# Kernel optimization log

Hardware: AMD Instinct MI355X
Metric: run time of the kernel (lower is better)

## Reference

```python
import math
import jax, jax.numpy as jnp
import numpy as np

B, T, E, H, A, NF = 8, 512, 1024, 16, 64, 64
HS = E // H
MLP = 4 * E

def _sinpos(t, dim):
    half = dim // 2
    freqs = jnp.exp(-math.log(10000.0) / (half - 1) * jnp.arange(half, dtype=jnp.float32))
    args = t.astype(jnp.float32)[:, None] * freqs[None, :]
    return jnp.concatenate([jnp.sin(args), jnp.cos(args)], axis=-1)

def _ada_ln(x, temb, w, b):
    # DiT-style adaLN: shift/scale modulate the normed x, alpha gates the branch
    h = jax.nn.silu(temb) @ w + b                      # [B, 3E]
    shift, scale, alpha = jnp.split(h, 3, axis=-1)
    mu = jnp.mean(x, axis=-1, keepdims=True)
    var = jnp.var(x, axis=-1, keepdims=True)
    xn = (x - mu) * jax.lax.rsqrt(var + 1e-5)
    return xn * (1.0 + scale[:, None, :]) + shift[:, None, :], alpha[:, None, :]

def _split_heads(x):
    b, n, c = x.shape
    return x.reshape(b, n, H, c // H).transpose(0, 2, 1, 3)

def _agent_attn(q, k, v, agents, qw, qb, kw, kb, vw, vb, ow, ob):
    # two-stage agent attention: agents attend to k/v, then q attends to agent context
    hs = q.shape[-1]
    inv = 1.0 / math.sqrt(hs)
    qa = agents[0] @ qw + qb                           # [H, A, hs] (shared across batch)
    ka = k @ kw + kb                                   # [B, H, N, hs]
    va = v @ vw + vb
    s1 = jax.nn.softmax(jnp.einsum('hax,bhnx->bhan', qa, ka) * inv, axis=-1)
    c1 = jnp.einsum('bhan,bhnx->bhax', s1, va)         # [B, H, A, hs]
    s2 = jax.nn.softmax(jnp.einsum('bhnx,bhax->bhna', q, c1) * inv, axis=-1)
    c2 = jnp.einsum('bhna,bhax->bhnx', s2, c1)         # [B, H, N, hs]
    b, h, n, _ = c2.shape
    return c2.transpose(0, 2, 1, 3).reshape(b, n, h * hs) @ ow + ob

def _conv1d(x, w, b):
    y = jax.lax.conv_general_dilated(x, w, (1,), [(1, 1)],
                                     dimension_numbers=('NCH', 'OIH', 'NCH'))
    return y + b[None, :, None]

def _fourier(x, low_freq=1, factor=1):
    b, t, d = x.shape
    xf = jnp.fft.rfft(x, axis=1)
    if t % 2 == 0:
        xf = xf[:, low_freq:-1]
        f = jnp.fft.rfftfreq(t)[low_freq:-1]
    else:
        xf = xf[:, low_freq:]
        f = jnp.fft.rfftfreq(t)[low_freq:]
    k = int(factor * math.log(xf.shape[1]))
    _, idx = jax.lax.top_k(jnp.moveaxis(jnp.abs(xf), 1, -1), k)    # [b, d, k]
    idx = jnp.moveaxis(idx, -1, 1)                                 # [b, k, d]
    xf_top = jnp.take_along_axis(xf, idx, axis=1)                  # [b, k, d] complex
    f_top = f.astype(jnp.float32)[idx]                             # [b, k, d]
    xf2 = jnp.concatenate([xf_top, jnp.conj(xf_top)], axis=1)      # [b, 2k, d]
    f2 = jnp.concatenate([f_top, -f_top], axis=1)[:, :, None, :]
    tt = jnp.arange(t, dtype=jnp.float32)[None, None, :, None]
    amp = jnp.abs(xf2)[:, :, None, :]
    phase = jnp.angle(xf2)[:, :, None, :]
    return jnp.sum(amp * jnp.cos(2.0 * math.pi * f2 * tt + phase), axis=1)

def _forward(x, encoder_output, timestep,
             ln1_w, ln1_b, ln11_w, ln11_b, ln2_w, ln2_b,
             a1_qkv_w, a1_qkv_b, a1_agq_w, a1_agq_b, a1_agk_w, a1_agk_b,
             a1_agv_w, a1_agv_b, a1_ago_w, a1_ago_b, a1_agents, a1_proj_w, a1_proj_b,
             a2_q_w, a2_q_b, a2_kv_w, a2_kv_b, a2_agq_w, a2_agq_b, a2_agk_w, a2_agk_b,
             a2_agv_w, a2_agv_b, a2_ago_w, a2_ago_b, a2_agents, a2_proj_w, a2_proj_b,
             tr_c1_w, tr_c1_b, tr_c2_w, tr_c2_b,
             mlp_w1, mlp_b1, mlp_w2, mlp_b2,
             pr_w, pr_b, lin_w, lin_b):
    temb = _sinpos(timestep, E)
    # self-attention (FullAttention with agent bottleneck)
    n1, al1 = _ada_ln(x, temb, ln1_w, ln1_b)
    q, k, v = jnp.split(n1 @ a1_qkv_w + a1_qkv_b, 3, axis=-1)
    y = _agent_attn(_split_heads(q), _split_heads(k), _split_heads(v), a1_agents,
                    a1_agq_w, a1_agq_b, a1_agk_w, a1_agk_b, a1_agv_w, a1_agv_b,
                    a1_ago_w, a1_ago_b)
    x = x + al1 * (y @ a1_proj_w + a1_proj_b)
    # cross-attention
    n11, al11 = _ada_ln(x, temb, ln11_w, ln11_b)
    qc = n11 @ a2_q_w + a2_q_b
    kc, vc = jnp.split(encoder_output @ a2_kv_w + a2_kv_b, 2, axis=-1)
    y = _agent_attn(_split_heads(qc), _split_heads(kc), _split_heads(vc), a2_agents,
                    a2_agq_w, a2_agq_b, a2_agk_w, a2_agk_b, a2_agv_w, a2_agv_b,
                    a2_ago_w, a2_ago_b)
    x = x + al11 * (y @ a2_proj_w + a2_proj_b)
    # 1x1 conv over channel dim (n_channel) then split into trend/seasonal inputs
    p = jnp.einsum('bce,oc->boe', x, pr_w) + pr_b[None, :, None]
    x1, x2 = jnp.split(p, 2, axis=1)
    h = jax.nn.gelu(_conv1d(x1, tr_c1_w, tr_c1_b), approximate=False)   # [B, 3, E]
    h = _conv1d(h.transpose(0, 2, 1), tr_c2_w, tr_c2_b)                 # [B, NF, 3]
    lin = jnp.arange(1, T + 1, dtype=jnp.float32) / (T + 1)
    poly = jnp.stack([lin ** (p_ + 1) for p_ in range(3)], axis=0)      # [3, T]
    trend = jnp.einsum('bnp,pt->btn', h, poly)                          # [B, T, NF]
    # seasonal branch: top-k Fourier extrapolation
    season = _fourier(x2)
    # MLP
    n2, al2 = _ada_ln(x, temb, ln2_w, ln2_b)
    mlp = jax.nn.gelu(n2 @ mlp_w1 + mlp_b1, approximate=False) @ mlp_w2 + mlp_b2
    x = x + al2 * mlp
    m = jnp.mean(x, axis=1, keepdims=True)
    return (x - m, m @ lin_w + lin_b, trend, season)

def setup_inputs():
    ks = iter(jax.random.split(jax.random.key(0), 64))
    def nrm(shape, s=0.02):
        return jax.random.normal(next(ks), shape, dtype=jnp.float32) * s
    z = lambda *s: jnp.zeros(s, jnp.float32)
    return dict(
        x=nrm((B, T, E), 1.0),
        encoder_output=nrm((B, T, E), 1.0),
        timestep=jax.random.randint(next(ks), (B,), 0, 1000),
        ln1_w=nrm((E, 3 * E)), ln1_b=z(3 * E),
        ln11_w=nrm((E, 3 * E)), ln11_b=z(3 * E),
        ln2_w=nrm((E, 3 * E)), ln2_b=z(3 * E),
        a1_qkv_w=nrm((E, 3 * E)), a1_qkv_b=z(3 * E),
        a1_agq_w=nrm((HS, HS)), a1_agq_b=z(HS),
        a1_agk_w=nrm((HS, HS)), a1_agk_b=z(HS),
        a1_agv_w=nrm((HS, HS)), a1_agv_b=z(HS),
        a1_ago_w=nrm((E, E)), a1_ago_b=z(E),
        a1_agents=nrm((1, H, A, HS), 1.0),
        a1_proj_w=nrm((E, E)), a1_proj_b=z(E),
        a2_q_w=nrm((E, E)), a2_q_b=z(E),
        a2_kv_w=nrm((E, 2 * E)), a2_kv_b=z(2 * E),
        a2_agq_w=nrm((HS, HS)), a2_agq_b=z(HS),
        a2_agk_w=nrm((HS, HS)), a2_agk_b=z(HS),
        a2_agv_w=nrm((HS, HS)), a2_agv_b=z(HS),
        a2_ago_w=nrm((E, E)), a2_ago_b=z(E),
        a2_agents=nrm((1, H, A, HS), 1.0),
        a2_proj_w=nrm((E, E)), a2_proj_b=z(E),
        tr_c1_w=nrm((3, T, 3)), tr_c1_b=z(3),
        tr_c2_w=nrm((NF, E, 3)), tr_c2_b=z(NF),
        mlp_w1=nrm((E, MLP)), mlp_b1=z(MLP),
        mlp_w2=nrm((MLP, E)), mlp_b2=z(E),
        pr_w=nrm((2 * T, T)), pr_b=z(2 * T),
        lin_w=nrm((E, NF)), lin_b=z(NF),
    )

def reference(x, encoder_output, timestep,
              ln1_w, ln1_b, ln11_w, ln11_b, ln2_w, ln2_b,
              a1_qkv_w, a1_qkv_b, a1_agq_w, a1_agq_b, a1_agk_w, a1_agk_b,
              a1_agv_w, a1_agv_b, a1_ago_w, a1_ago_b, a1_agents, a1_proj_w, a1_proj_b,
              a2_q_w, a2_q_b, a2_kv_w, a2_kv_b, a2_agq_w, a2_agq_b, a2_agk_w, a2_agk_b,
              a2_agv_w, a2_agv_b, a2_ago_w, a2_ago_b, a2_agents, a2_proj_w, a2_proj_b,
              tr_c1_w, tr_c1_b, tr_c2_w, tr_c2_b,
              mlp_w1, mlp_b1, mlp_w2, mlp_b2,
              pr_w, pr_b, lin_w, lin_b):
    return _forward(x, encoder_output, timestep,
                    ln1_w, ln1_b, ln11_w, ln11_b, ln2_w, ln2_b,
                    a1_qkv_w, a1_qkv_b, a1_agq_w, a1_agq_b, a1_agk_w, a1_agk_b,
                    a1_agv_w, a1_agv_b, a1_ago_w, a1_ago_b, a1_agents, a1_proj_w, a1_proj_b,
                    a2_q_w, a2_q_b, a2_kv_w, a2_kv_b, a2_agq_w, a2_agq_b, a2_agk_w, a2_agk_b,
                    a2_agv_w, a2_agv_b, a2_ago_w, a2_ago_b, a2_agents, a2_proj_w, a2_proj_b,
                    tr_c1_w, tr_c1_b, tr_c2_w, tr_c2_b,
                    mlp_w1, mlp_b1, mlp_w2, mlp_b2,
                    pr_w, pr_b, lin_w, lin_b)
```

## Files before the change

kernel.cpp:

```cpp
#include <hip/hip_runtime.h>
#include <hip/hip_bf16.h>

using bf16 = __hip_bfloat16;
typedef __attribute__((ext_vector_type(8))) short short8;
typedef __attribute__((ext_vector_type(4))) float floatx4;

constexpr int kB = 8, kT = 512, kE = 1024, kH = 16, kA = 64, kNF = 64, kHS = 64;
constexpr int kMLP = 4096, kT2 = 1024, kNFREQ = 255, kKTOP = 5;

constexpr int TAG_F32 = 0, TAG_BF16 = 1, TAG_AUTO = 2;

constexpr long BOFF_XC    = 0;
constexpr long BOFF_SMALL = 16777216;
constexpr long BOFF_FLAG  = 21137408;
constexpr long BOFF_WREG  = 21137472;
constexpr long BOFF_ACT   = 42108992;
constexpr long WS_NEED    = BOFF_ACT + 67108864;

constexpr long WR_Q   = 0;
constexpr long WR_KV  = 4194304;
constexpr long WR_AGO = 12582912;
constexpr long WR_PRJ = 16777216;
constexpr long WR_W1  = 0;
constexpr long WR_W2  = 8388608;

constexpr long AC_N1   = 0;
constexpr long AC_QBUF = 16777216;
constexpr long AC_KV   = 33554432;
constexpr long AC_KA   = 0;
constexpr long AC_VA   = 8388608;
constexpr long AC_ATT  = 33554432;
constexpr long AC_Y2   = 50331648;
constexpr long AC_P    = 0;
constexpr long AC_RE   = 33554432;
constexpr long AC_IM   = 41910272;
constexpr long AC_N1B  = 0;
constexpr long AC_HID  = 8388608;

constexpr long F_TS = 0, F_AD1 = 8192, F_AD11 = 32768, F_AD2 = 57344, F_QA = 81920,
               F_C1 = 147456, F_H2 = 671744, F_G1 = 673280, F_MB = 697856,
               F_TRE = 706048, F_TIM = 747008, F_TIX = 787968, F_TRIG = 828928;

constexpr long O0 = 0, O1 = 4194304, O2 = 4194816, O3 = 4456960;

__device__ inline float bf2f(bf16 h) {
    unsigned short u = *(unsigned short*)&h;
    return __uint_as_float((unsigned)u << 16);
}
__device__ inline unsigned short bfbits(bf16 b) { return *(unsigned short*)&b; }
__device__ inline float gelu_f(float x) {
    return 0.5f * x * (1.0f + erff(x * 0.7071067811865476f));
}
__device__ inline float4 load4f(const float* p) { return *(const float4*)p; }
__device__ inline float4 load4bf(const bf16* p) {
    ushort4 u = *(const ushort4*)p;
    float4 r;
    r.x = __uint_as_float((unsigned)u.x << 16);
    r.y = __uint_as_float((unsigned)u.y << 16);
    r.z = __uint_as_float((unsigned)u.z << 16);
    r.w = __uint_as_float((unsigned)u.w << 16);
    return r;
}
__device__ inline float4 load4auto(const void* p, long idx, bool isF32) {
    if (isF32) return load4f((const float*)p + idx);
    return load4bf((const bf16*)p + idx);
}
__device__ inline float ld1auto(const void* p, long idx, bool isF32) {
    if (isF32) return ((const float*)p)[idx];
    return bf2f(((const bf16*)p)[idx]);
}
__device__ inline void st1auto(void* p, long idx, bool isF32, float v) {
    if (isF32) ((float*)p)[idx] = v;
    else       ((bf16*)p)[idx] = __float2bfloat16(v);
}
__device__ inline float ldc1(const float* p) { return *p; }
__device__ inline float ldc1(const bf16* p) { return bf2f(*p); }
__device__ inline void stc1(float* p, float v) { *p = v; }
__device__ inline void stc1(bf16* p, float v) { *p = __float2bfloat16(v); }

__device__ inline void blockReduce2(float& a, float& b, float* sm) {
    #pragma unroll
    for (int m = 32; m > 0; m >>= 1) { a += __shfl_down(a, m); b += __shfl_down(b, m); }
    int w = threadIdx.x >> 6;
    if ((threadIdx.x & 63) == 0) { sm[w] = a; sm[4 + w] = b; }
    __syncthreads();
    a = sm[0] + sm[1] + sm[2] + sm[3];
    b = sm[4] + sm[5] + sm[6] + sm[7];
    __syncthreads();
}

__global__ void k_detect(const unsigned short* __restrict__ xraw, int* __restrict__ flag) {
    int tid = threadIdx.x;
    unsigned short h = xraw[2 * tid];
    float v = __uint_as_float((unsigned)h << 16);
    float av = fabsf(v);
    if (!(av == av)) av = 1e30f;
    __shared__ float red[4];
    for (int m = 32; m > 0; m >>= 1) av = fmaxf(av, __shfl_down(av, m));
    if ((tid & 63) == 0) red[tid >> 6] = av;
    __syncthreads();
    if (tid == 0) {
        float mx = fmaxf(fmaxf(red[0], red[1]), fmaxf(red[2], red[3]));
        flag[0] = (mx < 1e3f) ? 0 : 1;
    }
}

__global__ void k_temb(const int* __restrict__ ts, float* __restrict__ out) {
    int b = blockIdx.x, i = threadIdx.x;
    float t = (float)ts[b];
    const float rate = (float)(-9.210340371976184 / 511.0);
    float f = expf(rate * (float)i);
    float arg = t * f;
    float sv = sinf(arg), cv = cosf(arg);
    out[(long)b * kE + i]        = sv / (1.f + expf(-sv));
    out[(long)b * kE + 512 + i]  = cv / (1.f + expf(-cv));
}

__global__ void k_castin(const void* __restrict__ in, float* __restrict__ out,
                         const int* __restrict__ DF) {
    bool f = DF[0] != 0;
    long i = ((long)blockIdx.x * 256 + threadIdx.x) * 4;
    float4 v = load4auto(in, i, f);
    *(float4*)(out + i) = v;
}

__global__ __launch_bounds__(256) void k_wtf(const void* __restrict__ W, float* __restrict__ WT,
                                             int K, int Ntot, int c0,
                                             const int* __restrict__ DF) {
    bool f = DF[0] != 0;
    __shared__ float tile[32][33];
    int n0 = blockIdx.x * 32, k0 = blockIdx.y * 32;
    int tx = threadIdx.x & 31, ty = threadIdx.x >> 5;
    #pragma unroll
    for (int i = 0; i < 4; i++) {
        int k = ty + i * 8;
        tile[k][tx] = ld1auto(W, (long)(k0 + k) * Ntot + c0 + n0 + tx, f);
    }
    __syncthreads();
    #pragma unroll
    for (int i = 0; i < 4; i++) {
        int n = ty + i * 8;
        WT[(long)(n0 + n) * K + k0 + tx] = tile[tx][n];
    }
}

__global__ __launch_bounds__(256) void k_wt(const void* __restrict__ W, bf16* __restrict__ WT,
                                            int K, int N, const int* __restrict__ DF) {
    bool f = DF[0] != 0;
    __shared__ float tile[32][33];
    int n0 = blockIdx.x * 32, k0 = blockIdx.y * 32;
    int tx = threadIdx.x & 31, ty = threadIdx.x >> 5;
    #pragma unroll
    for (int i = 0; i < 4; i++) {
        int k = ty + i * 8;
        tile[k][tx] = ld1auto(W, (long)(k0 + k) * N + n0 + tx, f);
    }
    __syncthreads();
    #pragma unroll
    for (int i = 0; i < 4; i++) {
        int n = ty + i * 8;
        WT[(long)(n0 + n) * K + k0 + tx] = __float2bfloat16(tile[tx][n]);
    }
}

__global__ __launch_bounds__(256) void k_adalnf(const float* __restrict__ X,
                                                const float* __restrict__ AD,
                                                float* __restrict__ N) {
    int row = blockIdx.x;
    int b = row / kT;
    const float* xr = X + (long)row * kE;
    int tid = threadIdx.x;
    float4 xv = *(const float4*)(xr + tid * 4);
    float s  = xv.x + xv.y + xv.z + xv.w;
    float sq = xv.x * xv.x + xv.y * xv.y + xv.z * xv.z + xv.w * xv.w;
    __shared__ float sm[8];
    blockReduce2(s, sq, sm);
    float mu  = s * (1.f / kE);
    float var = sq * (1.f / kE) - mu * mu;
    float rstd = rsqrtf(fmaxf(var, 0.f) + 1e-5f);
    const float* ad = AD + (long)b * 3 * kE;
    float* nr = N + (long)row * kE;
    float xs[4] = {xv.x, xv.y, xv.z, xv.w};
    #pragma unroll
    for (int j = 0; j < 4; j++) {
        int e = tid * 4 + j;
        float xn = (xs[j] - mu) * rstd;
        nr[e] = xn * (1.f + ad[kE + e]) + ad[e];
    }
}

__global__ __launch_bounds__(256) void k_adaln(const float* __restrict__ X,
                                               const float* __restrict__ AD,
                                               bf16* __restrict__ N) {
    int row = blockIdx.x;
    int b = row / kT;
    const float* xr = X + (long)row * kE;
    int tid = threadIdx.x;
    float4 xv = *(const float4*)(xr + tid * 4);
    float s  = xv.x + xv.y + xv.z + xv.w;
    float sq = xv.x * xv.x + xv.y * xv.y + xv.z * xv.z + xv.w * xv.w;
    __shared__ float sm[8];
    blockReduce2(s, sq, sm);
    float mu  = s * (1.f / kE);
    float var = sq * (1.f / kE) - mu * mu;
    float rstd = rsqrtf(fmaxf(var, 0.f) + 1e-5f);
    const float* ad = AD + (long)b * 3 * kE;
    bf16* nr = N + (long)row * kE;
    float xs[4] = {xv.x, xv.y, xv.z, xv.w};
    #pragma unroll
    for (int j = 0; j < 4; j++) {
        int e = tid * 4 + j;
        float xn = (xs[j] - mu) * rstd;
        nr[e] = __float2bfloat16(xn * (1.f + ad[kE + e]) + ad[e]);
    }
}

template <typename TC>
__global__ __launch_bounds__(256) void k_mfma32(
    const float* __restrict__ A, int lda,
    const float* __restrict__ WT,
    TC* __restrict__ C, int ldc,
    int M, int N, int K,
    const void* __restrict__ bias, int bTag, long biasOff,
    const float* __restrict__ alpha, int alphaStride, int rowsPerB,
    const int* __restrict__ DF) {
    constexpr int BK = 32, PAD = 8;
    __shared__ bf16 Ah[128][BK + PAD], Al[128][BK + PAD];
    __shared__ bf16 Bh[128][BK + PAD], Bl[128][BK + PAD];
    int tid = threadIdx.x;
    int wave = tid >> 6, lane = tid & 63;
    int bm = blockIdx.y * 128, bn = blockIdx.x * 128;
    int wm = (wave >> 1) * 64, wn = (wave & 1) * 64;
    int lm = lane & 15, quad = lane >> 4;
    floatx4 acc[4][4] = {};
    int sRow = tid >> 1, sCol = (tid & 1) * 16;
    const float* ag = A  + (long)(bm + sRow) * lda + sCol;
    const float* bg = WT + (long)(bn + sRow) * K   + sCol;
    for (int k0 = 0; k0 < K; k0 += BK) {
        #pragma unroll
        for (int i = 0; i < 4; i++) {
            float4 v = *(const float4*)(ag + k0 + i * 4);
            bf16 h0 = __float2bfloat16(v.x), h1 = __float2bfloat16(v.y);
            bf16 h2 = __float2bfloat16(v.z), h3 = __float2bfloat16(v.w);
            bf16 l0 = __float2bfloat16(v.x - bf2f(h0));
            bf16 l1 = __float2bfloat16(v.y - bf2f(h1));
            bf16 l2 = __float2bfloat16(v.z - bf2f(h2));
            bf16 l3 = __float2bfloat16(v.w - bf2f(h3));
            ushort4 hv = {bfbits(h0), bfbits(h1), bfbits(h2), bfbits(h3)};
            ushort4 lv = {bfbits(l0), bfbits(l1), bfbits(l2), bfbits(l3)};
            *(ushort4*)&Ah[sRow][sCol + i * 4] = hv;
            *(ushort4*)&Al[sRow][sCol + i * 4] = lv;
        }
        #pragma unroll
        for (int i = 0; i < 4; i++) {
            float4 v = *(const float4*)(bg + k0 + i * 4);
            bf16 h0 = __float2bfloat16(v.x), h1 = __float2bfloat16(v.y);
            bf16 h2 = __float2bfloat16(v.z), h3 = __float2bfloat16(v.w);
            bf16 l0 = __float2bfloat16(v.x - bf2f(h0));
            bf16 l1 = __float2bfloat16(v.y - bf2f(h1));
            bf16 l2 = __float2bfloat16(v.z - bf2f(h2));
            bf16 l3 = __float2bfloat16(v.w - bf2f(h3));
            ushort4 hv = {bfbits(h0), bfbits(h1), bfbits(h2), bfbits(h3)};
            ushort4 lv = {bfbits(l0), bfbits(l1), bfbits(l2), bfbits(l3)};
            *(ushort4*)&Bh[sRow][sCol + i * 4] = hv;
            *(ushort4*)&Bl[sRow][sCol + i * 4] = lv;
        }
        __syncthreads();
        short8 ahf[4], alf[4], bhf[4], blf[4];
        #pragma unroll
        for (int mi = 0; mi < 4; mi++) {
            ahf[mi] = *(const short8*)&Ah[wm + mi * 16 + lm][quad * 8];
            alf[mi] = *(const short8*)&Al[wm + mi * 16 + lm][quad * 8];
        }
        #pragma unroll
        for (int ni = 0; ni < 4; ni++) {
            bhf[ni] = *(const short8*)&Bh[wn + ni * 16 + lm][quad * 8];
            blf[ni] = *(const short8*)&Bl[wn + ni * 16 + lm][quad * 8];
        }
        #pragma unroll
        for (int mi = 0; mi < 4; mi++)
            #pragma unroll
            for (int ni = 0; ni < 4; ni++) {
                acc[mi][ni] = __builtin_amdgcn_mfma_f32_16x16x32_bf16(ahf[mi], bhf[ni], acc[mi][ni], 0, 0, 0);
                acc[mi][ni] = __builtin_amdgcn_mfma_f32_16x16x32_bf16(ahf[mi], blf[ni], acc[mi][ni], 0, 0, 0);
                acc[mi][ni] = __builtin_amdgcn_mfma_f32_16x16x32_bf16(alf[mi], bhf[ni], acc[mi][ni], 0, 0, 0);
            }
        __syncthreads();
    }
    bool f32f = DF[0] != 0;
    bool bF = (bTag == TAG_F32) || (bTag == TAG_AUTO && f32f);
    #pragma unroll
    for (int ni = 0; ni < 4; ni++) {
        int col = bn + wn + ni * 16 + lm;
        float cb = bias ? ld1auto(bias, biasOff + col, bF) : 0.f;
        #pragma unroll
        for (int mi = 0; mi < 4; mi++) {
            #pragma unroll
            for (int reg = 0; reg < 4; reg++) {
                int row = bm + wm + mi * 16 + quad * 4 + reg;
                float v = acc[mi][ni][reg] + cb;
                TC* cp = C + (long)row * ldc + col;
                if (alpha) {
                    const float* al = alpha + (long)(row / rowsPerB) * alphaStride + col;
                    v = ldc1(cp) + al[0] * v;
                }
                stc1(cp, v);
            }
        }
    }
}

template <typename TC>
static void mgemm32(hipStream_t s, const float* A, int lda, const float* WT,
                    TC* C, int ldc, int M, int N, int K,
                    const void* bias, int bTag, long biasOff,
                    const float* alpha, int alphaStride, int rowsPerB, const int* DF) {
    dim3 g(N / 128, M / 128);
    k_mfma32<TC><<<g, 256, 0, s>>>(A, lda, WT, C, ldc, M, N, K,
                                   bias, bTag, biasOff, alpha, alphaStride, rowsPerB, DF);
}

template <typename TC>
__global__ __launch_bounds__(256) void k_mfma(
    const bf16* __restrict__ A, int lda,
    const bf16* __restrict__ WT,
    TC* __restrict__ C, int ldc,
    int M, int N, int K,
    const void* __restrict__ bias, int bTag, int act,
    const float* __restrict__ alpha, int alphaStride, int rowsPerB,
    const int* __restrict__ DF) {
    constexpr int BK = 64, PAD = 8;
    __shared__ bf16 As[128][BK + PAD];
    __shared__ bf16 Bs[128][BK + PAD];
    int tid = threadIdx.x;
    int wave = tid >> 6, lane = tid & 63;
    int bm = blockIdx.y * 128, bn = blockIdx.x * 128;
    int wm = (wave >> 1) * 64, wn = (wave & 1) * 64;
    int lm = lane & 15, quad = lane >> 4;
    floatx4 acc[4][4] = {};
    int sRow = tid >> 1, sCol = (tid & 1) * 32;
    const bf16* ag = A  + (long)(bm + sRow) * lda + sCol;
    const bf16* bg = WT + (long)(bn + sRow) * K   + sCol;
    for (int k0 = 0; k0 < K; k0 += BK) {
        #pragma unroll
        for (int i = 0; i < 4; i++)
            *(float4*)&As[sRow][sCol + i * 8] = *(const float4*)(ag + k0 + i * 8);
        #pragma unroll
        for (int i = 0; i < 4; i++)
            *(float4*)&Bs[sRow][sCol + i * 8] = *(const float4*)(bg + k0 + i * 8);
        __syncthreads();
        #pragma unroll
        for (int kk = 0; kk < BK; kk += 32) {
            short8 af[4], bf[4];
            #pragma unroll
            for (int mi = 0; mi < 4; mi++)
                af[mi] = *(const short8*)&As[wm + mi * 16 + lm][kk + quad * 8];
            #pragma unroll
            for (int ni = 0; ni < 4; ni++)
                bf[ni] = *(const short8*)&Bs[wn + ni * 16 + lm][kk + quad * 8];
            #pragma unroll
            for (int mi = 0; mi < 4; mi++)
                #pragma unroll
                for (int ni = 0; ni < 4; ni++)
                    acc[mi][ni] = __builtin_amdgcn_mfma_f32_16x16x32_bf16(
                        af[mi], bf[ni], acc[mi][ni], 0, 0, 0);
        }
        __syncthreads();
    }
    bool f32f = DF[0] != 0;
    bool bF = (bTag == TAG_F32) || (bTag == TAG_AUTO && f32f);
    #pragma unroll
    for (int ni = 0; ni < 4; ni++) {
        int col = bn + wn + ni * 16 + lm;
        float cb = bias ? ld1auto(bias, col, bF) : 0.f;
        #pragma unroll
        for (int mi = 0; mi < 4; mi++) {
            #pragma unroll
            for (int reg = 0; reg < 4; reg++) {
                int row = bm + wm + mi * 16 + quad * 4 + reg;
                float v = acc[mi][ni][reg] + cb;
                TC* cp = C + (long)row * ldc + col;
                if (alpha) {
                    const float* al = alpha + (long)(row / rowsPerB) * alphaStride + col;
                    v = ldc1(cp) + al[0] * v;
                } else if (act == 1) {
                    v = gelu_f(v);
                }
                stc1(cp, v);
            }
        }
    }
}

template <typename TC>
static void mgemm(hipStream_t s, const bf16* A, int lda, const bf16* WT,
                  TC* C, int ldc, int M, int N, int K,
                  const void* bias, int bTag, int act,
                  const float* alpha, int alphaStride, int rowsPerB, const int* DF) {
    dim3 g(N / 128, M / 128);
    k_mfma<TC><<<g, 256, 0, s>>>(A, lda, WT, C, ldc, M, N, K,
                                 bias, bTag, act, alpha, alphaStride, rowsPerB, DF);
}

template <typename TC>
__global__ __launch_bounds__(256) void k_gemm(
    const void* __restrict__ Ab, int aTag, int lda, long bsA,
    const void* __restrict__ Wb, int wTag, int ldw, long bsW,
    TC* __restrict__ Cb, int ldc, long bsC,
    int M, int N, int K,
    const void* __restrict__ bias, int bTag, int biasRow, int act,
    const float* __restrict__ alpha, int alphaStride, int rowsPerB,
    const int* __restrict__ DF) {
    __shared__ float As[16][68];
    __shared__ float Bs[16][68];
    bool f32f = DF[0] != 0;
    bool aF = (aTag == TAG_F32) || (aTag == TAG_AUTO && f32f);
    bool wF = (wTag == TAG_F32) || (wTag == TAG_AUTO && f32f);
    bool bF = (bTag == TAG_F32) || (bTag == TAG_AUTO && f32f);
    TC* Cbase = Cb + (long)blockIdx.z * bsC;
    long aBase = (long)blockIdx.z * bsA;
    long wBase = (long)blockIdx.z * bsW;
    int tid = threadIdx.x;
    int bm = blockIdx.y, bn = blockIdx.x;
    int tx = tid & 15, ty = tid >> 4;
    int arow = tid >> 2, acol = (tid & 3) * 4;
    int wrow = tid >> 4, wcol = (tid & 15) * 4;
    int gArow = bm * 64 + arow;
    bool aValid = gArow < M;
    float acc[4][4] = {};
    for (int kk = 0; kk < K; kk += 16) {
        float4 av = {0.f, 0.f, 0.f, 0.f};
        if (aValid) av = load4auto(Ab, aBase + (long)gArow * lda + kk + acol, aF);
        As[acol + 0][arow] = av.x;
        As[acol + 1][arow] = av.y;
        As[acol + 2][arow] = av.z;
        As[acol + 3][arow] = av.w;
        float4 wv = load4auto(Wb, wBase + (long)(kk + wrow) * ldw + bn * 64 + wcol, wF);
        *(float4*)&Bs[wrow][wcol] = wv;
        __syncthreads();
        #pragma unroll
        for (int k = 0; k < 16; k++) {
            float4 a4 = *(const float4*)&As[k][ty * 4];
            float4 b4 = *(const float4*)&Bs[k][tx * 4];
            acc[0][0] += a4.x * b4.x; acc[0][1] += a4.x * b4.y; acc[0][2] += a4.x * b4.z; acc[0][3] += a4.x * b4.w;
            acc[1][0] += a4.y * b4.x; acc[1][1] += a4.y * b4.y; acc[1][2] += a4.y * b4.z; acc[1][3] += a4.y * b4.w;
            acc[2][0] += a4.z * b4.x; acc[2][1] += a4.z * b4.y; acc[2][2] += a4.z * b4.z; acc[2][3] += a4.z * b4.w;
            acc[3][0] += a4.w * b4.x; acc[3][1] += a4.w * b4.y; acc[3][2] += a4.w * b4.z; acc[3][3] += a4.w * b4.w;
        }
        __syncthreads();
    }
    int gcol = bn * 64 + tx * 4;
    float cb[4] = {0.f, 0.f, 0.f, 0.f};
    if (bias && !biasRow) {
        #pragma unroll
        for (int j = 0; j < 4; j++) cb[j] = ld1auto(bias, gcol + j, bF);
    }
    #pragma unroll
    for (int i = 0; i < 4; i++) {
        int grow = bm * 64 + ty * 4 + i;
        if (grow >= M) continue;
        float rb = (bias && biasRow) ? ld1auto(bias, grow, bF) : 0.f;
        TC* crow = Cbase + (long)grow * ldc + gcol;
        const float* al = nullptr;
        if (alpha) al = alpha + (long)(grow / rowsPerB) * alphaStride + gcol;
        #pragma unroll
        for (int j = 0; j < 4; j++) {
            float v = acc[i][j] + cb[j] + rb;
            if (alpha)         v = ldc1(crow + j) + al[j] * v;
            else if (act == 1) v = gelu_f(v);
            stc1(crow + j, v);
        }
    }
}

template <typename TC>
static void gemm(hipStream_t s, const void* A, int aTag, int lda, long bsA,
                 const void* W, int wTag, int ldw, long bsW,
                 TC* C, int ldc, long bsC, int M, int N, int K,
                 const void* bias, int bTag, int biasRow, int act,
                 const float* alpha, int alphaStride, int rowsPerB, int batch,
                 const int* DF) {
    dim3 g(N / 64, (M + 63) / 64, batch);
    k_gemm<TC><<<g, 256, 0, s>>>(A, aTag, lda, bsA, W, wTag, ldw, bsW, C, ldc, bsC,
                                 M, N, K, bias, bTag, biasRow, act,
                                 alpha, alphaStride, rowsPerB, DF);
}

__global__ __launch_bounds__(256) void k_agatt1(const float* __restrict__ qa,
                                                const bf16* __restrict__ ka,
                                                const bf16* __restrict__ va,
                                                float* __restrict__ c1) {
    int blk = blockIdx.x;
    int a = blk % kA;
    int h = (blk / kA) % kH;
    int b = blk / (kA * kH);
    __shared__ float qrow[kHS];
    __shared__ float probs[kT];
    __shared__ float sm[8];
    __shared__ float part[4][64];
    int tid = threadIdx.x;
    if (tid < kHS) qrow[tid] = qa[((long)h * kA + a) * kHS + tid];
    __syncthreads();
    const bf16* kab = ka + ((long)h * kB + b) * kT * kHS;
    float sc[2];
    #pragma unroll
    for (int rep = 0; rep < 2; rep++) {
        const bf16* kr = kab + (long)(tid + rep * 256) * kHS;
        float acc = 0.f;
        #pragma unroll
        for (int d = 0; d < kHS; d += 4) {
            float4 k4 = load4bf(kr + d);
            acc += k4.x * qrow[d] + k4.y * qrow[d + 1] + k4.z * qrow[d + 2] + k4.w * qrow[d + 3];
        }
        sc[rep] = acc * 0.125f;
    }
    float mx = fmaxf(sc[0], sc[1]);
    for (int m = 32; m > 0; m >>= 1) mx = fmaxf(mx, __shfl_down(mx, m));
    if ((tid & 63) == 0) sm[tid >> 6] = mx;
    __syncthreads();
    mx = fmaxf(fmaxf(sm[0], sm[1]), fmaxf(sm[2], sm[3]));
    float e0 = expf(sc[0] - mx), e1 = expf(sc[1] - mx);
    float ss = e0 + e1;
    for (int m = 32; m > 0; m >>= 1) ss += __shfl_down(ss, m);
    if ((tid & 63) == 0) sm[4 + (tid >> 6)] = ss;
    __syncthreads();
    ss = sm[4] + sm[5] + sm[6] + sm[7];
    float rs = 1.f / ss;
    probs[tid] = e0 * rs;
    probs[tid + 256] = e1 * rs;
    __syncthreads();
    int d = tid & 63, ch = tid >> 6;
    const bf16* vab = va + ((long)h * kB + b) * kT * kHS;
    float acc = 0.f;
    for (int n = ch * 128; n < (ch + 1) * 128; n++)
        acc += probs[n] * bf2f(vab[(long)n * kHS + d]);
    part[ch][d] = acc;
    __syncthreads();
    if (tid < 64)
        c1[(((long)b * kH + h) * kA + a) * kHS + tid] =
            part[0][tid] + part[1][tid] + part[2][tid] + part[3][tid];
}

__global__ __launch_bounds__(256) void k_agatt2f(const float* __restrict__ qsrc, int ldq,
                                                 const float* __restrict__ c1,
                                                 float* __restrict__ out) {
    int blk = blockIdx.x;
    int nt = blk % (kT / 16);
    int h = (blk / (kT / 16)) % kH;
    int b = blk / ((kT / 16) * kH);
    __shared__ float c1s[kA][kHS + 1];
    __shared__ float qs[16][kHS + 1];
    __shared__ float ps[16][kA + 1];
    int tid = threadIdx.x;
    const float* c1b = c1 + ((long)b * kH + h) * kA * kHS;
    for (int i = tid; i < kA * kHS; i += 256) c1s[i >> 6][i & 63] = c1b[i];
    int n0 = nt * 16;
    {
        int r = tid >> 4, d = (tid & 15) * 4;
        float4 q4 = load4f(qsrc + (long)(b * kT + n0 + r) * ldq + h * kHS + d);
        qs[r][d] = q4.x; qs[r][d + 1] = q4.y; qs[r][d + 2] = q4.z; qs[r][d + 3] = q4.w;
    }
    __syncthreads();
    int r = tid >> 4, c = tid & 15;
    float sc[4];
    #pragma unroll
    for (int j = 0; j < 4; j++) {
        int a = c * 4 + j;
        float acc = 0.f;
        for (int d = 0; d < kHS; d++) acc += qs[r][d] * c1s[a][d];
        sc[j] = acc * 0.125f;
    }
    float mx = fmaxf(fmaxf(sc[0], sc[1]), fmaxf(sc[2], sc[3]));
    for (int m = 1; m < 16; m <<= 1) mx = fmaxf(mx, __shfl_xor(mx, m));
    float e[4], ss = 0.f;
    #pragma unroll
    for (int j = 0; j < 4; j++) { e[j] = expf(sc[j] - mx); ss += e[j]; }
    for (int m = 1; m < 16; m <<= 1) ss += __shfl_xor(ss, m);
    float rs = 1.f / ss;
    #pragma unroll
    for (int j = 0; j < 4; j++) ps[r][c * 4 + j] = e[j] * rs;
    __syncthreads();
    float o0 = 0.f, o1 = 0.f, o2 = 0.f, o3 = 0.f;
    int d0 = c * 4;
    for (int a = 0; a < kA; a++) {
        float p = ps[r][a];
        o0 += p * c1s[a][d0 + 0];
        o1 += p * c1s[a][d0 + 1];
        o2 += p * c1s[a][d0 + 2];
        o3 += p * c1s[a][d0 + 3];
    }
    float* orow = out + (long)(b * kT + n0 + r) * kE + h * kHS + d0;
    orow[0] = o0; orow[1] = o1; orow[2] = o2; orow[3] = o3;
}

__global__ void k_trig(float* __restrict__ trig) {
    int id = blockIdx.x * 256 + threadIdx.x;
    if (id >= kNFREQ * kT) return;
    int t = id & 511;
    int f = (id >> 9) + 1;
    int m = (f * t) & 511;
    double ang = (double)m * (2.0 * 3.14159265358979323846 / 512.0);
    trig[id] = (float)cos(ang);
    trig[kNFREQ * kT + id] = (float)(-sin(ang));
}

__global__ __launch_bounds__(256) void k_topk(const float* __restrict__ RE, const float* __restrict__ IM,
                                              float* __restrict__ tre, float* __restrict__ tim,
                                              int* __restrict__ tix) {
    int tid = threadIdx.x;
    int c = tid & 15;
    int j = tid >> 4;
    int colId = blockIdx.x * 16 + c;
    int b = colId >> 10, e = colId & 1023;
    const float* rp = RE + (long)b * kNFREQ * kE + e;
    const float* ip = IM + (long)b * kNFREQ * kE + e;
    float bv[kKTOP] = {-1e30f, -1e30f, -1e30f, -1e30f, -1e30f};
    int bi[kKTOP] = {1 << 30, 1 << 30, 1 << 30, 1 << 30, 1 << 30};
    #pragma unroll
    for (int s = 0; s < 16; s++) {
        int fq = j * 16 + s;
        if (fq >= kNFREQ) break;
        float re = rp[(long)fq * kE], im = ip[(long)fq * kE];
        float m2 = re * re + im * im;
        if (m2 > bv[kKTOP - 1] || (m2 == bv[kKTOP - 1] && fq < bi[kKTOP - 1])) {
            int p = kKTOP - 1;
            while (p > 0 && (m2 > bv[p - 1] || (m2 == bv[p - 1] && fq < bi[p - 1]))) {
                bv[p] = bv[p - 1]; bi[p] = bi[p - 1]; p--;
            }
            bv[p] = m2; bi[p] = fq;
        }
    }
    __shared__ float sv[16][16][kKTOP];
    __shared__ int   si[16][16][kKTOP];
    #pragma unroll
    for (int q = 0; q < kKTOP; q++) { sv[c][j][q] = bv[q]; si[c][j][q] = bi[q]; }
    __syncthreads();
    if (j == 0) {
        for (int jj = 1; jj < 16; jj++) {
            #pragma unroll
            for (int q = 0; q < kKTOP; q++) {
                float v = sv[c][jj][q];
                int fq = si[c][jj][q];
                if (v > bv[kKTOP - 1] || (v == bv[kKTOP - 1] && fq < bi[kKTOP - 1])) {
                    int p = kKTOP - 1;
                    while (p > 0 && (v > bv[p - 1] || (v == bv[p - 1] && fq < bi[p - 1]))) {
                        bv[p] = bv[p - 1]; bi[p] = bi[p - 1]; p--;
                    }
                    bv[p] = v; bi[p] = fq;
                }
            }
        }
        #pragma unroll
        for (int q = 0; q < kKTOP; q++) {
            int fq = bi[q];
            tre[(long)colId * kKTOP + q] = rp[(long)fq * kE];
            tim[(long)colId * kKTOP + q] = ip[(long)fq * kE];
            tix[(long)colId * kKTOP + q] = fq;
        }
    }
}

__global__ void k_season(const float* __restrict__ tre, const float* __restrict__ tim,
                         const int* __restrict__ tix, const float* __restrict__ trig,
                         void* __restrict__ out, long obase, const int* __restrict__ DF) {
    bool f32o = DF[0] != 0;
    long id = (long)blockIdx.x * 256 + threadIdx.x;
    int e = id & 1023;
    long bt = id >> 10;
    int t = (int)(bt & 511);
    int b = (int)(bt >> 9);
    long be = (long)b * kE + e;
    float acc = 0.f;
    #pragma unroll
    for (int j = 0; j < kKTOP; j++) {
        int f = tix[be * kKTOP + j];
        acc += tre[be * kKTOP + j] * trig[(long)f * kT + t]
             + tim[be * kKTOP + j] * trig[(long)kNFREQ * kT + (long)f * kT + t];
    }
    st1auto(out, obase + id, f32o, 2.f * acc);
}

__global__ __launch_bounds__(256) void k_conv1(const float* __restrict__ P,
                                               const void* __restrict__ w,
                                               const void* __restrict__ bias,
                                               float* __restrict__ G,
                                               const int* __restrict__ DF) {
    bool f = DF[0] != 0;
    int bo = blockIdx.x;
    int lt = blockIdx.y;
    int o = bo % 3, b = bo / 3;
    int tid = threadIdx.x;
    __shared__ float ws[512][3];
    for (int idx = tid; idx < 512 * 3; idx += 256)
        ws[idx / 3][idx % 3] = ld1auto(w, (long)o * 512 * 3 + idx, f);
    __syncthreads();
    int l = lt * 128 + (tid & 127);
    int ih = (tid >> 7) * 256;
    const float* xb = P + (long)b * kT2 * kE;
    float acc = 0.f;
    for (int ii = 0; ii < 256; ii++) {
        int i = ih + ii;
        const float* xr = xb + (long)i * kE + l;
        float xm = (l > 0)    ? xr[-1] : 0.f;
        float xc = xr[0];
        float xp = (l < 1023) ? xr[1]  : 0.f;
        acc += xm * ws[i][0] + xc * ws[i][1] + xp * ws[i][2];
    }
    __shared__ float red[128];
    if (tid >= 128) red[tid - 128] = acc;
    __syncthreads();
    if (tid < 128) {
        float tot = acc + red[tid] + ld1auto(bias, o, f);
        G[((long)b * 3 + o) * 1024 + l] = gelu_f(tot);
    }
}

__global__ __launch_bounds__(256) void k_conv2(const float* __restrict__ G,
                                               const void* __restrict__ w,
                                               const void* __restrict__ bias,
                                               float* __restrict__ H2,
                                               const int* __restrict__ DF) {
    bool f = DF[0] != 0;
    int n = blockIdx.x % kNF;
    int b = blockIdx.x / kNF;
    int tid = threadIdx.x;
    const float* Gb = G + (long)b * 3 * 1024;
    float a0 = 0.f, a1 = 0.f, a2 = 0.f;
    for (int i = tid; i < 1024; i += 256) {
        float g0 = Gb[i], g1 = Gb[1024 + i], g2 = Gb[2048 + i];
        long wo = ((long)n * 1024 + i) * 3;
        float w0 = ld1auto(w, wo + 0, f);
        float w1 = ld1auto(w, wo + 1, f);
        float w2 = ld1auto(w, wo + 2, f);
        a0 += g0 * w1 + g1 * w2;
        a1 += g0 * w0 + g1 * w1 + g2 * w2;
        a2 += g1 * w0 + g2 * w1;
    }
    __shared__ float sm[12];
    #pragma unroll
    for (int m = 32; m > 0; m >>= 1) {
        a0 += __shfl_down(a0, m);
        a1 += __shfl_down(a1, m);
        a2 += __shfl_down(a2, m);
    }
    int wv = tid >> 6;
    if ((tid & 63) == 0) { sm[wv] = a0; sm[4 + wv] = a1; sm[8 + wv] = a2; }
    __syncthreads();
    if (tid == 0) {
        float cb = ld1auto(bias, n, f);
        float* hp = H2 + ((long)b * kNF + n) * 3;
        hp[0] = cb + sm[0] + sm[1] + sm[2] + sm[3];
        hp[1] = cb + sm[4] + sm[5] + sm[6] + sm[7];
        hp[2] = cb + sm[8] + sm[9] + sm[10] + sm[11];
    }
}

__global__ void k_trend(const float* __restrict__ H2, void* __restrict__ out, long obase,
                        const int* __restrict__ DF) {
    bool f32o = DF[0] != 0;
    int id = blockIdx.x * 256 + threadIdx.x;
    int n = id % kNF;
    int t = (id / kNF) % kT;
    int b = id / (kNF * kT);
    float lin = (float)(t + 1) / 513.0f;
    const float* h = H2 + ((long)b * kNF + n) * 3;
    float l2 = lin * lin;
    st1auto(out, obase + id, f32o, h[0] * lin + h[1] * l2 + h[2] * l2 * lin);
}

__global__ void k_mean(const float* __restrict__ X, float* __restrict__ m) {
    int id = blockIdx.x * 256 + threadIdx.x;
    int b = id >> 10, e = id & 1023;
    const float* p = X + (long)b * kT * kE + e;
    float s = 0.f;
    for (int t = 0; t < kT; t++) s += p[(long)t * kE];
    m[id] = s * (1.f / kT);
}

__global__ void k_out0(const float* __restrict__ X, const float* __restrict__ m,
                       void* __restrict__ out, long obase, const int* __restrict__ DF) {
    bool f32o = DF[0] != 0;
    long id = (long)blockIdx.x * 256 + threadIdx.x;
    int e = id & 1023;
    int b = (int)(id >> 19);
    st1auto(out, obase + id, f32o, X[id] - m[b * kE + e]);
}

__global__ void k_out1(const float* __restrict__ m, const void* __restrict__ w,
                       const void* __restrict__ bias, void* __restrict__ out, long obase,
                       const int* __restrict__ DF) {
    bool f = DF[0] != 0;
    int id = blockIdx.x * 256 + threadIdx.x;
    if (id >= kB * kNF) return;
    int b = id / kNF, n = id % kNF;
    float acc = ld1auto(bias, n, f);
    for (int e = 0; e < kE; e++) acc += m[b * kE + e] * ld1auto(w, (long)e * kNF + n, f);
    st1auto(out, obase + id, f, acc);
}

extern "C" void kernel_launch(void* const* d_in, const int* in_sizes, int n_in,
                              void* d_out, int out_size, void* d_ws, size_t ws_size,
                              hipStream_t stream) {
    (void)in_sizes; (void)n_in; (void)out_size; (void)ws_size;
    const void* x_in = d_in[0];
    const void* enc  = d_in[1];
    const int* tstep = (const int*)d_in[2];
    const void *ln1_w = d_in[3],  *ln1_b = d_in[4],  *ln11_w = d_in[5], *ln11_b = d_in[6];
    const void *ln2_w = d_in[7],  *ln2_b = d_in[8];
    const void *a1_qkv_w = d_in[9], *a1_qkv_b = d_in[10];
    const void *a1_agq_w = d_in[11], *a1_agq_b = d_in[12];
    const void *a1_agk_w = d_in[13], *a1_agk_b = d_in[14];
    const void *a1_agv_w = d_in[15], *a1_agv_b = d_in[16];
    const void *a1_ago_w = d_in[17], *a1_ago_b = d_in[18];
    const void *a1_agents = d_in[19];
    const void *a1_proj_w = d_in[20], *a1_proj_b = d_in[21];
    const void *a2_q_w = d_in[22], *a2_q_b = d_in[23];
    const void *a2_kv_w = d_in[24], *a2_kv_b = d_in[25];
    const void *a2_agq_w = d_in[26], *a2_agq_b = d_in[27];
    const void *a2_agk_w = d_in[28], *a2_agk_b = d_in[29];
    const void *a2_agv_w = d_in[30], *a2_agv_b = d_in[31];
    const void *a2_ago_w = d_in[32], *a2_ago_b = d_in[33];
    const void *a2_agents = d_in[34];
    const void *a2_proj_w = d_in[35], *a2_proj_b = d_in[36];
    const void *tr_c1_w = d_in[37], *tr_c1_b = d_in[38];
    const void *tr_c2_w = d_in[39], *tr_c2_b = d_in[40];
    const void *mlp_w1 = d_in[41], *mlp_b1 = d_in[42];
    const void *mlp_w2 = d_in[43], *mlp_b2 = d_in[44];
    const void *pr_w = d_in[45], *pr_b = d_in[46];
    const void *lin_w = d_in[47], *lin_b = d_in[48];

    char* wsb = (char*)d_ws;
    float* XC = (float*)(wsb + BOFF_XC);
    float* SM = (float*)(wsb + BOFF_SMALL);
    float* TS = SM + F_TS;
    float* AD1 = SM + F_AD1;
    float* AD11 = SM + F_AD11;
    float* AD2 = SM + F_AD2;
    float* QA = SM + F_QA;
    float* C1 = SM + F_C1;
    float* H2 = SM + F_H2;
    float* G1 = SM + F_G1;
    float* MB = SM + F_MB;
    float* TRE = SM + F_TRE;
    float* TIM = SM + F_TIM;
    int*   TIX = (int*)(SM + F_TIX);
    float* TRIG = SM + F_TRIG;
    int* DF = (int*)(wsb + BOFF_FLAG);
    char* WR = wsb + BOFF_WREG;
    float* WTQ  = (float*)(WR + WR_Q);
    float* WTKV = (float*)(WR + WR_KV);
    float* WAGO = (float*)(WR + WR_AGO);
    float* WPRJ = (float*)(WR + WR_PRJ);
    bf16*  W1B  = (bf16*)(WR + WR_W1);
    bf16*  W2B  = (bf16*)(WR + WR_W2);
    char* AC = wsb + BOFF_ACT;
    float* N1F  = (float*)(AC + AC_N1);
    float* QBUF = (float*)(AC + AC_QBUF);
    float* KVB  = (float*)(AC + AC_KV);
    bf16*  KA   = (bf16*)(AC + AC_KA);
    bf16*  VA   = (bf16*)(AC + AC_VA);
    float* ATTF = (float*)(AC + AC_ATT);
    float* Y2F  = (float*)(AC + AC_Y2);
    float* P    = (float*)(AC + AC_P);
    float* RE   = (float*)(AC + AC_RE);
    float* IM   = (float*)(AC + AC_IM);
    bf16*  N1B  = (bf16*)(AC + AC_N1B);
    bf16*  HID  = (bf16*)(AC + AC_HID);

    const int M_BT = kB * kT;
    const long bsKA = (long)kB * kT * kHS;

    k_detect<<<1, 256, 0, stream>>>((const unsigned short*)x_in, DF);

    k_wtf<<<dim3(1024/32, 1024/32), 256, 0, stream>>>(a1_qkv_w, WTQ, 1024, 3072, 0, DF);
    k_wtf<<<dim3(2048/32, 1024/32), 256, 0, stream>>>(a1_qkv_w, WTKV, 1024, 3072, 1024, DF);
    k_wtf<<<dim3(1024/32, 1024/32), 256, 0, stream>>>(a1_ago_w, WAGO, 1024, 1024, 0, DF);
    k_wtf<<<dim3(1024/32, 1024/32), 256, 0, stream>>>(a1_proj_w, WPRJ, 1024, 1024, 0, DF);

    k_temb<<<kB, 512, 0, stream>>>(tstep, TS);
    gemm(stream, TS, TAG_F32, kE, 0L, ln1_w, TAG_AUTO, 3 * kE, 0L, AD1, 3 * kE, 0L,
         kB, 3 * kE, kE, ln1_b, TAG_AUTO, 0, 0, nullptr, 0, 1, 1, DF);
    gemm(stream, TS, TAG_F32, kE, 0L, ln11_w, TAG_AUTO, 3 * kE, 0L, AD11, 3 * kE, 0L,
         kB, 3 * kE, kE, ln11_b, TAG_AUTO, 0, 0, nullptr, 0, 1, 1, DF);
    gemm(stream, TS, TAG_F32, kE, 0L, ln2_w, TAG_AUTO, 3 * kE, 0L, AD2, 3 * kE, 0L,
         kB, 3 * kE, kE, ln2_b, TAG_AUTO, 0, 0, nullptr, 0, 1, 1, DF);
    k_castin<<<(kB * kT * kE) / 1024, 256, 0, stream>>>(x_in, XC, DF);
    k_trig<<<(kNFREQ * kT + 255) / 256, 256, 0, stream>>>(TRIG);

    k_adalnf<<<M_BT, 256, 0, stream>>>(XC, AD1, N1F);
    mgemm32(stream, N1F, kE, WTQ, QBUF, kE, M_BT, kE, kE,
            a1_qkv_b, TAG_AUTO, 0L, nullptr, 0, 1, DF);
    mgemm32(stream, N1F, kE, WTKV, KVB, 2 * kE, M_BT, 2 * kE, kE,
            a1_qkv_b, TAG_AUTO, (long)kE, nullptr, 0, 1, DF);
    gemm(stream, a1_agents, TAG_AUTO, kHS, 0L, a1_agq_w, TAG_AUTO, kHS, 0L, QA, kHS, 0L,
         kH * kA, kHS, kHS, a1_agq_b, TAG_AUTO, 0, 0, nullptr, 0, 1, 1, DF);
    gemm(stream, KVB, TAG_F32, 2 * kE, 64L, a1_agk_w, TAG_AUTO, kHS, 0L, KA, kHS, bsKA,
         M_BT, kHS, kHS, a1_agk_b, TAG_AUTO, 0, 0, nullptr, 0, 1, kH, DF);
    gemm(stream, KVB + kE, TAG_F32, 2 * kE, 64L, a1_agv_w, TAG_AUTO, kHS, 0L, VA, kHS, bsKA,
         M_BT, kHS, kHS, a1_agv_b, TAG_AUTO, 0, 0, nullptr, 0, 1, kH, DF);
    k_agatt1<<<kB * kH * kA, 256, 0, stream>>>(QA, KA, VA, C1);
    k_agatt2f<<<kB * kH * (kT / 16), 256, 0, stream>>>(QBUF, kE, C1, ATTF);
    mgemm32(stream, ATTF, kE, WAGO, Y2F, kE, M_BT, kE, kE,
            a1_ago_b, TAG_AUTO, 0L, nullptr, 0, 1, DF);
    mgemm32(stream, Y2F, kE, WPRJ, XC, kE, M_BT, kE, kE,
            a1_proj_b, TAG_AUTO, 0L, AD1 + 2 * kE, 3 * kE, kT, DF);

    k_wtf<<<dim3(1024/32, 1024/32), 256, 0, stream>>>(a2_q_w, WTQ, 1024, 1024, 0, DF);
    k_wtf<<<dim3(2048/32, 1024/32), 256, 0, stream>>>(a2_kv_w, WTKV, 1024, 2048, 0, DF);
    k_wtf<<<dim3(1024/32, 1024/32), 256, 0, stream>>>(a2_ago_w, WAGO, 1024, 1024, 0, DF);
    k_wtf<<<dim3(1024/32, 1024/32), 256, 0, stream>>>(a2_proj_w, WPRJ, 1024, 1024, 0, DF);

    k_castin<<<(kB * kT * kE) / 1024, 256, 0, stream>>>(enc, N1F, DF);
    mgemm32(stream, N1F, kE, WTKV, KVB, 2 * kE, M_BT, 2 * kE, kE,
            a2_kv_b, TAG_AUTO, 0L, nullptr, 0, 1, DF);
    k_adalnf<<<M_BT, 256, 0, stream>>>(XC, AD11, N1F);
    mgemm32(stream, N1F, kE, WTQ, QBUF, kE, M_BT, kE, kE,
            a2_q_b, TAG_AUTO, 0L, nullptr, 0, 1, DF);
    gemm(stream, a2_agents, TAG_AUTO, kHS, 0L, a2_agq_w, TAG_AUTO, kHS, 0L, QA, kHS, 0L,
         kH * kA, kHS, kHS, a2_agq_b, TAG_AUTO, 0, 0, nullptr, 0, 1, 1, DF);
    gemm(stream, KVB, TAG_F32, 2 * kE, 64L, a2_agk_w, TAG_AUTO, kHS, 0L, KA, kHS, bsKA,
         M_BT, kHS, kHS, a2_agk_b, TAG_AUTO, 0, 0, nullptr, 0, 1, kH, DF);
    gemm(stream, KVB + kE, TAG_F32, 2 * kE, 64L, a2_agv_w, TAG_AUTO, kHS, 0L, VA, kHS, bsKA,
         M_BT, kHS, kHS, a2_agv_b, TAG_AUTO, 0, 0, nullptr, 0, 1, kH, DF);
    k_agatt1<<<kB * kH * kA, 256, 0, stream>>>(QA, KA, VA, C1);
    k_agatt2f<<<kB * kH * (kT / 16), 256, 0, stream>>>(QBUF, kE, C1, ATTF);
    mgemm32(stream, ATTF, kE, WAGO, Y2F, kE, M_BT, kE, kE,
            a2_ago_b, TAG_AUTO, 0L, nullptr, 0, 1, DF);
    mgemm32(stream, Y2F, kE, WPRJ, XC, kE, M_BT, kE, kE,
            a2_proj_b, TAG_AUTO, 0L, AD11 + 2 * kE, 3 * kE, kT, DF);

    gemm(stream, pr_w, TAG_AUTO, kT, 0L, XC, TAG_F32, kE, (long)kT * kE,
         P, kE, (long)kT2 * kE, kT2, kE, kT,
         pr_b, TAG_AUTO, 1, 0, nullptr, 0, 1, kB, DF);
    gemm(stream, TRIG, TAG_F32, kT, 0L, P + (long)kT * kE, TAG_F32, kE, (long)kT2 * kE,
         RE, kE, (long)kNFREQ * kE, kNFREQ, kE, kT,
         nullptr, 0, 0, 0, nullptr, 0, 1, kB, DF);
    gemm(stream, TRIG + (long)kNFREQ * kT, TAG_F32, kT, 0L, P + (long)kT * kE, TAG_F32, kE, (long)kT2 * kE,
         IM, kE, (long)kNFREQ * kE, kNFREQ, kE, kT,
         nullptr, 0, 0, 0, nullptr, 0, 1, kB, DF);
    k_topk<<<(kB * kE) / 16, 256, 0, stream>>>(RE, IM, TRE, TIM, TIX);
    k_season<<<(kB * kT * kE) / 256, 256, 0, stream>>>(TRE, TIM, TIX, TRIG, d_out, O3, DF);
    k_conv1<<<dim3(kB * 3, 8), 256, 0, stream>>>(P, tr_c1_w, tr_c1_b, G1, DF);
    k_conv2<<<kB * kNF, 256, 0, stream>>>(G1, tr_c2_w, tr_c2_b, H2, DF);
    k_trend<<<(kB * kT * kNF) / 256, 256, 0, stream>>>(H2, d_out, O2, DF);

    k_wt<<<dim3(4096/32, 1024/32), 256, 0, stream>>>(mlp_w1, W1B, 1024, 4096, DF);
    k_wt<<<dim3(1024/32, 4096/32), 256, 0, stream>>>(mlp_w2, W2B, 4096, 1024, DF);
    k_adaln<<<M_BT, 256, 0, stream>>>(XC, AD2, N1B);
    mgemm(stream, N1B, kE, W1B, HID, kMLP, M_BT, kMLP, kE,
          mlp_b1, TAG_AUTO, 1 , nullptr, 0, 1, DF);
    mgemm(stream, HID, kMLP, W2B, XC, kE, M_BT, kE, kMLP,
          mlp_b2, TAG_AUTO, 0, AD2 + 2 * kE, 3 * kE, kT, DF);

    k_mean<<<(kB * kE) / 256, 256, 0, stream>>>(XC, MB);
    k_out0<<<(kB * kT * kE) / 256, 256, 0, stream>>>(XC, MB, d_out, O0, DF);
    k_out1<<<(kB * kNF + 255) / 256, 256, 0, stream>>>(MB, lin_w, lin_b, d_out, O1, DF);
}
```

Before: 2.378 ms.

## Process four agents per block in agent attention stage one to reuse K/V loads

The first agent-attention kernel now handles four agent queries per block instead of one, so each K row and V row loaded from global memory is reused across four dot products and four weighted sums. The PV accumulation is reorganised into 16 row-chunks by 16 float4 column groups, with a shared-memory reduction across chunks. The grid shrinks by a factor of four. This cuts redundant K/V traffic in exchange for more registers and shared memory per block and fewer blocks in flight.

```diff
diff --git a/kernel.cpp b/kernel.cpp
--- a/kernel.cpp
+++ b/kernel.cpp
@@ -490,55 +490,105 @@
                                                 const bf16* __restrict__ ka,
                                                 const bf16* __restrict__ va,
                                                 float* __restrict__ c1) {
+    constexpr int AQ = 4;
     int blk = blockIdx.x;
-    int a = blk % kA;
-    int h = (blk / kA) % kH;
-    int b = blk / (kA * kH);
-    __shared__ float qrow[kHS];
-    __shared__ float probs[kT];
-    __shared__ float sm[8];
-    __shared__ float part[4][64];
+    int aq = blk % (kA / AQ);
+    int h = (blk / (kA / AQ)) % kH;
+    int b = blk / ((kA / AQ) * kH);
+    int ag0 = aq * AQ;
+    __shared__ float qs[AQ][kHS];
+    __shared__ float probs[AQ][kT];
+    __shared__ float red[16][AQ * 68];
+    __shared__ float sred[32];
     int tid = threadIdx.x;
-    if (tid < kHS) qrow[tid] = qa[((long)h * kA + a) * kHS + tid];
+    {
+        int ag = tid >> 6, d = tid & 63;
+        qs[ag][d] = qa[((long)h * kA + ag0 + ag) * kHS + d];
+    }
     __syncthreads();
     const bf16* kab = ka + ((long)h * kB + b) * kT * kHS;
-    float sc[2];
+    float sc[2][AQ];
     #pragma unroll
     for (int rep = 0; rep < 2; rep++) {
         const bf16* kr = kab + (long)(tid + rep * 256) * kHS;
-        float acc = 0.f;
+        float a0 = 0.f, a1 = 0.f, a2 = 0.f, a3 = 0.f;
         #pragma unroll
         for (int d = 0; d < kHS; d += 4) {
             float4 k4 = load4bf(kr + d);
-            acc += k4.x * qrow[d] + k4.y * qrow[d + 1] + k4.z * qrow[d + 2] + k4.w * qrow[d + 3];
-        }
-        sc[rep] = acc * 0.125f;
-    }
-    float mx = fmaxf(sc[0], sc[1]);
-    for (int m = 32; m > 0; m >>= 1) mx = fmaxf(mx, __shfl_down(mx, m));
-    if ((tid & 63) == 0) sm[tid >> 6] = mx;
-    __syncthreads();
-    mx = fmaxf(fmaxf(sm[0], sm[1]), fmaxf(sm[2], sm[3]));
-    float e0 = expf(sc[0] - mx), e1 = expf(sc[1] - mx);
-    float ss = e0 + e1;
-    for (int m = 32; m > 0; m >>= 1) ss += __shfl_down(ss, m);
-    if ((tid & 63) == 0) sm[4 + (tid >> 6)] = ss;
-    __syncthreads();
-    ss = sm[4] + sm[5] + sm[6] + sm[7];
-    float rs = 1.f / ss;
-    probs[tid] = e0 * rs;
-    probs[tid + 256] = e1 * rs;
-    __syncthreads();
-    int d = tid & 63, ch = tid >> 6;
+            float4 q0 = *(const float4*)&qs[0][d];
+            float4 q1 = *(const float4*)&qs[1][d];
+            float4 q2 = *(const float4*)&qs[2][d];
+            float4 q3 = *(const float4*)&qs[3][d];
+            a0 += k4.x * q0.x + k4.y * q0.y + k4.z * q0.z + k4.w * q0.w;
+            a1 += k4.x * q1.x + k4.y * q1.y + k4.z * q1.z + k4.w * q1.w;
+            a2 += k4.x * q2.x + k4.y * q2.y + k4.z * q2.z + k4.w * q2.w;
+            a3 += k4.x * q3.x + k4.y * q3.y + k4.z * q3.z + k4.w * q3.w;
+        }
+        sc[rep][0] = a0 * 0.125f; sc[rep][1] = a1 * 0.125f;
+        sc[rep][2] = a2 * 0.125f; sc[rep][3] = a3 * 0.125f;
+    }
+    int w = tid >> 6;
+    float mx[AQ], ss[AQ];
+    #pragma unroll
+    for (int ag = 0; ag < AQ; ag++) mx[ag] = fmaxf(sc[0][ag], sc[1][ag]);
+    #pragma unroll
+    for (int m = 32; m > 0; m >>= 1)
+        #pragma unroll
+        for (int ag = 0; ag < AQ; ag++) mx[ag] = fmaxf(mx[ag], __shfl_down(mx[ag], m));
+    if ((tid & 63) == 0)
+        #pragma unroll
+        for (int ag = 0; ag < AQ; ag++) sred[w * 4 + ag] = mx[ag];
+    __syncthreads();
+    #pragma unroll
+    for (int ag = 0; ag < AQ; ag++)
+        mx[ag] = fmaxf(fmaxf(sred[ag], sred[4 + ag]), fmaxf(sred[8 + ag], sred[12 + ag]));
+    float e0[AQ], e1[AQ];
+    #pragma unroll
+    for (int ag = 0; ag < AQ; ag++) {
+        e0[ag] = expf(sc[0][ag] - mx[ag]);
+        e1[ag] = expf(sc[1][ag] - mx[ag]);
+        ss[ag] = e0[ag] + e1[ag];
+    }
+    #pragma unroll
+    for (int m = 32; m > 0; m >>= 1)
+        #pragma unroll
+        for (int ag = 0; ag < AQ; ag++) ss[ag] += __shfl_down(ss[ag], m);
+    if ((tid & 63) == 0)
+        #pragma unroll
+        for (int ag = 0; ag < AQ; ag++) sred[16 + w * 4 + ag] = ss[ag];
+    __syncthreads();
+    #pragma unroll
+    for (int ag = 0; ag < AQ; ag++) {
+        float tot = sred[16 + ag] + sred[20 + ag] + sred[24 + ag] + sred[28 + ag];
+        float rs = 1.f / tot;
+        probs[ag][tid] = e0[ag] * rs;
+        probs[ag][tid + 256] = e1[ag] * rs;
+    }
+    __syncthreads();
+    int dg = tid & 15, nc = tid >> 4;
     const bf16* vab = va + ((long)h * kB + b) * kT * kHS;
-    float acc = 0.f;
-    for (int n = ch * 128; n < (ch + 1) * 128; n++)
-        acc += probs[n] * bf2f(vab[(long)n * kHS + d]);
-    part[ch][d] = acc;
-    __syncthreads();
-    if (tid < 64)
-        c1[(((long)b * kH + h) * kA + a) * kHS + tid] =
-            part[0][tid] + part[1][tid] + part[2][tid] + part[3][tid];
+    float4 acc[AQ] = {};
+    for (int s = 0; s < 32; s++) {
+        int n = nc * 32 + s;
+        float4 v = load4bf(vab + (long)n * kHS + dg * 4);
+        #pragma unroll
+        for (int ag = 0; ag < AQ; ag++) {
+            float p = probs[ag][n];
+            acc[ag].x += p * v.x; acc[ag].y += p * v.y;
+            acc[ag].z += p * v.z; acc[ag].w += p * v.w;
+        }
+    }
+    #pragma unroll
+    for (int ag = 0; ag < AQ; ag++)
+        *(float4*)&red[nc][ag * 68 + dg * 4] = acc[ag];
+    __syncthreads();
+    {
+        int ag = tid >> 6, d = tid & 63;
+        float s = 0.f;
+        #pragma unroll
+        for (int n2 = 0; n2 < 16; n2++) s += red[n2][ag * 68 + d];
+        c1[(((long)b * kH + h) * kA + ag0 + ag) * kHS + d] = s;
+    }
 }
 
 __global__ __launch_bounds__(256) void k_agatt2f(const float* __restrict__ qsrc, int ldq,
@@ -898,7 +948,7 @@
          M_BT, kHS, kHS, a1_agk_b, TAG_AUTO, 0, 0, nullptr, 0, 1, kH, DF);
     gemm(stream, KVB + kE, TAG_F32, 2 * kE, 64L, a1_agv_w, TAG_AUTO, kHS, 0L, VA, kHS, bsKA,
          M_BT, kHS, kHS, a1_agv_b, TAG_AUTO, 0, 0, nullptr, 0, 1, kH, DF);
-    k_agatt1<<<kB * kH * kA, 256, 0, stream>>>(QA, KA, VA, C1);
+    k_agatt1<<<kB * kH * (kA / 4), 256, 0, stream>>>(QA, KA, VA, C1);
     k_agatt2f<<<kB * kH * (kT / 16), 256, 0, stream>>>(QBUF, kE, C1, ATTF);
     mgemm32(stream, ATTF, kE, WAGO, Y2F, kE, M_BT, kE, kE,
             a1_ago_b, TAG_AUTO, 0L, nullptr, 0, 1, DF);
@@ -922,7 +972,7 @@
          M_BT, kHS, kHS, a2_agk_b, TAG_AUTO, 0, 0, nullptr, 0, 1, kH, DF);
     gemm(stream, KVB + kE, TAG_F32, 2 * kE, 64L, a2_agv_w, TAG_AUTO, kHS, 0L, VA, kHS, bsKA,
          M_BT, kHS, kHS, a2_agv_b, TAG_AUTO, 0, 0, nullptr, 0, 1, kH, DF);
-    k_agatt1<<<kB * kH * kA, 256, 0, stream>>>(QA, KA, VA, C1);
+    k_agatt1<<<kB * kH * (kA / 4), 256, 0, stream>>>(QA, KA, VA, C1);
     k_agatt2f<<<kB * kH * (kT / 16), 256, 0, stream>>>(QBUF, kE, C1, ATTF);
     mgemm32(stream, ATTF, kE, WAGO, Y2F, kE, M_BT, kE, kE,
             a2_ago_b, TAG_AUTO, 0L, nullptr, 0, 1, DF);
```

After: 2.230 ms. -6.2%, faster.
